# Kernel optimization log

Measured on AMD Instinct MI355X. Metric: run time of the kernel, lower is better.

The kernel has to match this reference:

```python
import jax, jax.numpy as jnp
import numpy as np

D_MODEL = 1024
NUM_HEADS = 16
KEY_DIM = 64
VALUE_DIM = 64
NEG_INF = jnp.float32(-1e30)


def setup_inputs() -> dict:
    key = jax.random.key(0)
    ks = jax.random.split(key, 10)
    B, S = 2, 2048
    lim = 1.0 / np.sqrt(D_MODEL)
    x = jax.random.normal(ks[0], (B, S, D_MODEL), dtype=jnp.float32)
    mask = jnp.ones((B, S), dtype=jnp.int32)  # pad mask: 1 = keep
    # stacked per-head linear params (Linear stores weight as [out, in])
    Wq = jax.random.uniform(ks[1], (NUM_HEADS, KEY_DIM, D_MODEL), jnp.float32, -lim, lim)
    bq = jax.random.uniform(ks[2], (NUM_HEADS, KEY_DIM), jnp.float32, -lim, lim)
    Wk = jax.random.uniform(ks[3], (NUM_HEADS, KEY_DIM, D_MODEL), jnp.float32, -lim, lim)
    bk = jax.random.uniform(ks[4], (NUM_HEADS, KEY_DIM), jnp.float32, -lim, lim)
    Wv = jax.random.uniform(ks[5], (NUM_HEADS, VALUE_DIM, D_MODEL), jnp.float32, -lim, lim)
    bv = jax.random.uniform(ks[6], (NUM_HEADS, VALUE_DIM), jnp.float32, -lim, lim)
    lim_o = 1.0 / np.sqrt(NUM_HEADS * VALUE_DIM)
    Wo = jax.random.uniform(ks[7], (D_MODEL, NUM_HEADS * VALUE_DIM), jnp.float32, -lim_o, lim_o)
    bo = jax.random.uniform(ks[8], (D_MODEL,), jnp.float32, -lim_o, lim_o)
    return {"x": x, "mask": mask, "Wq": Wq, "bq": bq, "Wk": Wk, "bk": bk,
            "Wv": Wv, "bv": bv, "Wo": Wo, "bo": bo}


def _mha(x, mask, Wq, bq, Wk, bk, Wv, bv, Wo, bo):
    B, S, _ = x.shape
    # per-head projections: [B, H, S, k]
    q = jnp.einsum('bsd,hkd->bhsk', x, Wq) + bq[None, :, None, :]
    k = jnp.einsum('bsd,hkd->bhsk', x, Wk) + bk[None, :, None, :]
    v = jnp.einsum('bsd,hvd->bhsv', x, Wv) + bv[None, :, None, :]
    scale = 1.0 / np.sqrt(KEY_DIM).astype(np.float32)
    scores = jnp.einsum('bhik,bhjk->bhij', q, k) * scale  # [B, H, S, S]
    # final mask = causal AND pad-row AND pad-col
    causal = jnp.tril(jnp.ones((S, S), dtype=bool))
    pad = mask.astype(bool)
    final = causal[None, None] & pad[:, None, :, None] & pad[:, None, None, :]
    masked = jnp.where(final, scores, NEG_INF)
    w = jax.nn.softmax(masked, axis=-1)
    w = jnp.where(final, w, 0.0)  # fully-masked rows -> zeros, matching loop impl
    out = jnp.einsum('bhij,bhjv->bhiv', w, v)            # [B, H, S, V]
    concat = out.transpose(0, 2, 1, 3).reshape(B, S, NUM_HEADS * VALUE_DIM)
    return concat @ Wo.T + bo


def reference(x, mask, Wq, bq, Wk, bk, Wv, bv, Wo, bo):
    return _mha(x, mask, Wq, bq, Wk, bk, Wv, bv, Wo, bo)
```

## Files before the change

kernel.cpp:

```cpp
#include <hip/hip_runtime.h>

#define SEQ 2048
#define NH 16
#define HD 64
#define DMODEL 1024

__device__ __forceinline__ unsigned int f2bf(float f) {
  unsigned int u = __float_as_uint(f);
  return ((u + 0x7fffu + ((u >> 16) & 1u)) >> 16) & 0xffffu;
}

__device__ __forceinline__ unsigned int pk2bf(float a, float b) {
  unsigned short ua = __builtin_bit_cast(unsigned short, (__bf16)a);
  unsigned short ub = __builtin_bit_cast(unsigned short, (__bf16)b);
  return (unsigned int)ua | ((unsigned int)ub << 16);
}

typedef __bf16 bf16x8 __attribute__((ext_vector_type(8)));
typedef float f32x4 __attribute__((ext_vector_type(4)));

__device__ __forceinline__ void gl2lds16(const unsigned short* g, unsigned short* l) {
  __builtin_amdgcn_global_load_lds(
      (const __attribute__((address_space(1))) unsigned int*)g,
      (__attribute__((address_space(3))) unsigned int*)l, 16, 0, 0);
}

__global__ __launch_bounds__(256) void cast_all_kernel(
    const float* __restrict__ x, const float* __restrict__ wq,
    const float* __restrict__ wk, const float* __restrict__ wv,
    const float* __restrict__ wo,
    unsigned short* __restrict__ xb, unsigned short* __restrict__ wqb,
    unsigned short* __restrict__ wkb, unsigned short* __restrict__ wvb,
    unsigned short* __restrict__ wob) {
  int idx = blockIdx.x * 256 + threadIdx.x;
  if (idx >= 1048576) return;
  const float* src;
  unsigned short* dst;
  int off;
  if (idx < 524288) {
    src = x; dst = xb; off = idx;
  } else {
    int t = idx - 524288;
    int w = t >> 17;
    off = t & 131071;
    src = (w == 0) ? wq : (w == 1) ? wk : (w == 2) ? wv : wo;
    dst = (w == 0) ? wqb : (w == 1) ? wkb : (w == 2) ? wvb : wob;
  }
  const float4* p = reinterpret_cast<const float4*>(src) + (size_t)off * 2;
  float4 a = p[0], b = p[1];
  uint4 o;
  o.x = f2bf(a.x) | (f2bf(a.y) << 16);
  o.y = f2bf(a.z) | (f2bf(a.w) << 16);
  o.z = f2bf(b.x) | (f2bf(b.y) << 16);
  o.w = f2bf(b.z) | (f2bf(b.w) << 16);
  reinterpret_cast<uint4*>(dst)[off] = o;
}

template <int MODE>
__global__ __launch_bounds__(256) void gemm128(
    const unsigned short* __restrict__ A, const unsigned short* __restrict__ B,
    const float* __restrict__ bias0, const float* __restrict__ bias1,
    const float* __restrict__ bias2, float* __restrict__ Cf,
    unsigned short* __restrict__ Qo, unsigned short* __restrict__ Ko,
    unsigned short* __restrict__ Vto, int Kdim) {
  __shared__ __align__(16) unsigned short As[128 * 64];
  __shared__ __align__(16) unsigned short Bs[128 * 64];
  const int tid = threadIdx.x;
  const int wave = tid >> 6, lane = tid & 63;
  const int wm = wave >> 1, wn = wave & 1;
  const int fr = lane & 15, quad = lane >> 4;
  const int fx = fr & 7;
  const int n0 = blockIdx.x * 128, m0 = blockIdx.y * 128;

  const int srowg = lane >> 3;
  const int schunk = (lane & 7) ^ (srowg & 7);
  const unsigned short* Abase =
      A + (size_t)(m0 + wave * 32 + srowg) * Kdim + schunk * 8;
  const unsigned short* Bbase =
      B + (size_t)(n0 + wave * 32 + srowg) * Kdim + schunk * 8;
  unsigned short* AsW = As + (wave * 32) * 64;
  unsigned short* BsW = Bs + (wave * 32) * 64;

  f32x4 acc[4][4];
#pragma unroll
  for (int mt = 0; mt < 4; ++mt)
#pragma unroll
    for (int nt = 0; nt < 4; ++nt) acc[mt][nt] = f32x4{0.f, 0.f, 0.f, 0.f};

  for (int k0 = 0; k0 < Kdim; k0 += 64) {
#pragma unroll
    for (int t = 0; t < 4; ++t) {
      gl2lds16(Abase + (size_t)(t * 8) * Kdim + k0, AsW + t * 8 * 64);
      gl2lds16(Bbase + (size_t)(t * 8) * Kdim + k0, BsW + t * 8 * 64);
    }
    __syncthreads();
#pragma unroll
    for (int ks = 0; ks < 2; ++ks) {
      bf16x8 af[4], bfv[4];
#pragma unroll
      for (int mt = 0; mt < 4; ++mt)
        af[mt] = *reinterpret_cast<const bf16x8*>(
            As + (wm * 64 + mt * 16 + fr) * 64 + ((ks * 4 + quad) ^ fx) * 8);
#pragma unroll
      for (int nt = 0; nt < 4; ++nt)
        bfv[nt] = *reinterpret_cast<const bf16x8*>(
            Bs + (wn * 64 + nt * 16 + fr) * 64 + ((ks * 4 + quad) ^ fx) * 8);
#pragma unroll
      for (int mt = 0; mt < 4; ++mt)
#pragma unroll
        for (int nt = 0; nt < 4; ++nt)
          acc[mt][nt] = __builtin_amdgcn_mfma_f32_16x16x32_bf16(
              af[mt], bfv[nt], acc[mt][nt], 0, 0, 0);
    }
    __syncthreads();
  }

  if (MODE == 0) {
    const int seg = n0 >> 10;
    const float* bp = (seg == 0) ? bias0 : (seg == 1) ? bias1 : bias2;
    const float scale = (seg == 0) ? 0.1803368809f : 1.0f;
    unsigned short* QK = (seg == 0) ? Qo : Ko;
#pragma unroll
    for (int nt = 0; nt < 4; ++nt) {
      const int c = (n0 + wn * 64 + nt * 16 + fr) & 1023;
      const int h = c >> 6, d = c & 63;
      const float bs = bp[c];
#pragma unroll
      for (int mt = 0; mt < 4; ++mt) {
        const int mbase = m0 + wm * 64 + mt * 16 + quad * 4;
        const int b = mbase >> 11, s0 = mbase & 2047;
        if (seg < 2) {
          unsigned short* dst = QK + (((size_t)(b * NH + h)) * SEQ + s0) * HD + d;
#pragma unroll
          for (int r = 0; r < 4; ++r)
            dst[(size_t)r * HD] = (unsigned short)f2bf((acc[mt][nt][r] + bs) * scale);
        } else {
          uint2 pk;
          pk.x = pk2bf(acc[mt][nt][0] + bs, acc[mt][nt][1] + bs);
          pk.y = pk2bf(acc[mt][nt][2] + bs, acc[mt][nt][3] + bs);
          *reinterpret_cast<uint2*>(
              Vto + (((size_t)(b * NH + h)) * HD + d) * SEQ + s0) = pk;
        }
      }
    }
  } else {
#pragma unroll
    for (int nt = 0; nt < 4; ++nt) {
      const int cg = n0 + wn * 64 + nt * 16 + fr;
      const float bs = bias0[cg];
#pragma unroll
      for (int mt = 0; mt < 4; ++mt) {
        const int mbase = m0 + wm * 64 + mt * 16 + quad * 4;
#pragma unroll
        for (int r = 0; r < 4; ++r)
          Cf[(size_t)(mbase + r) * DMODEL + cg] = acc[mt][nt][r] + bs;
      }
    }
  }
}

__global__ __launch_bounds__(256, 4) void attn_mfma_kernel(
    const unsigned short* __restrict__ Qg, const unsigned short* __restrict__ Kg,
    const unsigned short* __restrict__ Vtg, const int* __restrict__ mask,
    unsigned short* __restrict__ concat) {
  const int w = blockIdx.x >> 8;
  const int c = blockIdx.x & 255;
  const int gg = c >> 5;
  const int bh = c & 31;
  const int ib = (w == 0) ? (31 - gg) : (w == 1) ? gg : (w == 2) ? (23 - gg) : (8 + gg);
  const int b = bh >> 4, h = bh & 15;
  const int tid = threadIdx.x;
  const int wave = tid >> 6, lane = tid & 63;
  const int quad = lane >> 4, fr = lane & 15;
  const int fx = fr & 7;

  __shared__ __align__(16) unsigned short Ks[2][64 * 64];
  __shared__ __align__(16) unsigned short Vts[2][64 * 64];
  __shared__ __align__(16) unsigned short Pt[4][16 * 64];

  const unsigned short* Qb = Qg + ((size_t)bh * SEQ) * HD;
  const unsigned short* Kb = Kg + ((size_t)bh * SEQ) * HD;
  const unsigned short* Vtb = Vtg + ((size_t)bh * HD) * SEQ;
  const int* maskb = mask + b * SEQ;

  bool badl = false;
  {
    const int4* mp4 = reinterpret_cast<const int4*>(maskb);
#pragma unroll
    for (int u = 0; u < 8; ++u) {
      int4 v = mp4[lane * 8 + u];
      badl |= !(v.x && v.y && v.z && v.w);
    }
  }
  const unsigned long long bm = __ballot(badl);

  const int ir = ib * 64 + wave * 16 + fr;
  const bf16x8 q0 = *reinterpret_cast<const bf16x8*>(Qb + (size_t)ir * HD + quad * 8);
  const bf16x8 q1 = *reinterpret_cast<const bf16x8*>(Qb + (size_t)ir * HD + quad * 8 + 32);
  const int padi = maskb[ir];

  f32x4 o[4];
#pragma unroll
  for (int vt = 0; vt < 4; ++vt) o[vt] = f32x4{0.f, 0.f, 0.f, 0.f};
  float mr = -1e20f, lr = 0.f;

  const int srowg = lane >> 3;
  const int schunk = (lane & 7) ^ (srowg & 7);
  const unsigned short* Ksrc = Kb + (size_t)(wave * 16 + srowg) * HD + schunk * 8;
  const unsigned short* Vsrc = Vtb + (size_t)(wave * 16 + srowg) * SEQ + schunk * 8;
  const int cA0 = (quad ^ fx) * 8;
  const int cA1 = ((quad + 4) ^ fx) * 8;
  unsigned short* PtW = Pt[wave];

  {
    unsigned short* KsW = Ks[0] + (wave * 16) * 64;
    unsigned short* VtsW = Vts[0] + (wave * 16) * 64;
#pragma unroll
    for (int t = 0; t < 2; ++t) {
      gl2lds16(Ksrc + (size_t)(t * 8) * HD, KsW + t * 8 * 64);
      gl2lds16(Vsrc + (size_t)(t * 8) * SEQ, VtsW + t * 8 * 64);
    }
  }

  for (int jc = 0; jc <= ib; ++jc) {
    __syncthreads();
    if (jc < ib) {
      const int jn = (jc + 1) * 64;
      unsigned short* KsW = Ks[(jc + 1) & 1] + (wave * 16) * 64;
      unsigned short* VtsW = Vts[(jc + 1) & 1] + (wave * 16) * 64;
#pragma unroll
      for (int t = 0; t < 2; ++t) {
        gl2lds16(Ksrc + (size_t)(jn + t * 8) * HD, KsW + t * 8 * 64);
        gl2lds16(Vsrc + (size_t)(t * 8) * SEQ + jn, VtsW + t * 8 * 64);
      }
    }
    const unsigned short* Kcur = Ks[jc & 1];
    const unsigned short* Vcur = Vts[jc & 1];
    const int j0 = jc * 64;
    const bool tb = ((bm >> (2 * jc)) & 3ull) != 0ull;

    f32x4 st[4];
#pragma unroll
    for (int jt = 0; jt < 4; ++jt) {
      bf16x8 ka0 = *reinterpret_cast<const bf16x8*>(&Kcur[(jt * 16 + fr) * 64 + cA0]);
      bf16x8 ka1 = *reinterpret_cast<const bf16x8*>(&Kcur[(jt * 16 + fr) * 64 + cA1]);
      st[jt] = f32x4{0.f, 0.f, 0.f, 0.f};
      st[jt] = __builtin_amdgcn_mfma_f32_16x16x32_bf16(ka0, q0, st[jt], 0, 0, 0);
      st[jt] = __builtin_amdgcn_mfma_f32_16x16x32_bf16(ka1, q1, st[jt], 0, 0, 0);
    }

    if (tb) {
      const int4* mp = reinterpret_cast<const int4*>(maskb + j0);
#pragma unroll
      for (int jt = 0; jt < 4; ++jt) {
        const int4 mv = mp[jt * 4 + quad];
        if (mv.x == 0) st[jt][0] = -1e30f;
        if (mv.y == 0) st[jt][1] = -1e30f;
        if (mv.z == 0) st[jt][2] = -1e30f;
        if (mv.w == 0) st[jt][3] = -1e30f;
      }
    }
    if (jc == ib) {
#pragma unroll
      for (int jt = 0; jt < 4; ++jt) {
        const int jb = j0 + jt * 16 + quad * 4;
#pragma unroll
        for (int r = 0; r < 4; ++r)
          if (jb + r > ir) st[jt][r] = -1e30f;
      }
    }

    float tmax = -1e30f;
#pragma unroll
    for (int jt = 0; jt < 4; ++jt)
#pragma unroll
      for (int r = 0; r < 4; ++r) tmax = fmaxf(tmax, st[jt][r]);
    tmax = fmaxf(tmax, __shfl_xor(tmax, 16));
    tmax = fmaxf(tmax, __shfl_xor(tmax, 32));
    const bool upd = __ballot(tmax > mr) != 0ull;
    float corr = 1.f;
    if (upd) { const float mn = fmaxf(mr, tmax); corr = __builtin_amdgcn_exp2f(mr - mn); mr = mn; }
    float lloc = 0.f;
#pragma unroll
    for (int jt = 0; jt < 4; ++jt) {
      float p0 = __builtin_amdgcn_exp2f(st[jt][0] - mr);
      float p1 = __builtin_amdgcn_exp2f(st[jt][1] - mr);
      float p2 = __builtin_amdgcn_exp2f(st[jt][2] - mr);
      float p3 = __builtin_amdgcn_exp2f(st[jt][3] - mr);
      lloc += (p0 + p1) + (p2 + p3);
      uint2 pk; pk.x = pk2bf(p0, p1); pk.y = pk2bf(p2, p3);
      const int pc = (2 * jt + (quad >> 1)) ^ fx;
      *reinterpret_cast<uint2*>(&PtW[fr * 64 + pc * 8 + (quad & 1) * 4]) = pk;
    }
    lloc += __shfl_xor(lloc, 16);
    lloc += __shfl_xor(lloc, 32);
    if (upd) {
      lr = lr * corr + lloc;
#pragma unroll
      for (int vt = 0; vt < 4; ++vt) {
        o[vt][0] *= corr; o[vt][1] *= corr; o[vt][2] *= corr; o[vt][3] *= corr;
      }
    } else {
      lr += lloc;
    }

    bf16x8 pa0 = *reinterpret_cast<const bf16x8*>(&PtW[fr * 64 + (quad ^ fx) * 8]);
    bf16x8 pa1 = *reinterpret_cast<const bf16x8*>(&PtW[fr * 64 + ((quad + 4) ^ fx) * 8]);
#pragma unroll
    for (int vt = 0; vt < 4; ++vt) {
      bf16x8 vb0 = *reinterpret_cast<const bf16x8*>(&Vcur[(vt * 16 + fr) * 64 + cA0]);
      bf16x8 vb1 = *reinterpret_cast<const bf16x8*>(&Vcur[(vt * 16 + fr) * 64 + cA1]);
      o[vt] = __builtin_amdgcn_mfma_f32_16x16x32_bf16(vb0, pa0, o[vt], 0, 0, 0);
      o[vt] = __builtin_amdgcn_mfma_f32_16x16x32_bf16(vb1, pa1, o[vt], 0, 0, 0);
    }
  }

  const float inv = (padi != 0 && lr > 0.f) ? 1.f / lr : 0.f;
  unsigned short* orow = concat + ((size_t)(b * SEQ + ir)) * DMODEL + h * HD;
#pragma unroll
  for (int vt = 0; vt < 4; ++vt) {
    uint2 pk;
    pk.x = pk2bf(o[vt][0] * inv, o[vt][1] * inv);
    pk.y = pk2bf(o[vt][2] * inv, o[vt][3] * inv);
    *reinterpret_cast<uint2*>(orow + vt * 16 + quad * 4) = pk;
  }
}

extern "C" void kernel_launch(void* const* d_in, const int* in_sizes, int n_in,
                              void* d_out, int out_size, void* d_ws, size_t ws_size,
                              hipStream_t stream) {
  (void)in_sizes; (void)n_in; (void)out_size;
  const float* x  = (const float*)d_in[0];
  const int* mask = (const int*)d_in[1];
  const float* Wq = (const float*)d_in[2];
  const float* bq = (const float*)d_in[3];
  const float* Wk = (const float*)d_in[4];
  const float* bk = (const float*)d_in[5];
  const float* Wv = (const float*)d_in[6];
  const float* bv = (const float*)d_in[7];
  const float* Wo = (const float*)d_in[8];
  const float* bo = (const float*)d_in[9];
  float* out = (float*)d_out;

  char* ws = (char*)d_ws;
  if (ws_size < (48ull << 20)) return;
  unsigned short* xb  = (unsigned short*)(ws);
  unsigned short* wqb = (unsigned short*)(ws + (8ull  << 20));
  unsigned short* wkb = (unsigned short*)(ws + (10ull << 20));
  unsigned short* wvb = (unsigned short*)(ws + (12ull << 20));
  unsigned short* wob = (unsigned short*)(ws + (14ull << 20));
  unsigned short* Qb  = (unsigned short*)(ws + (16ull << 20));
  unsigned short* Kb  = (unsigned short*)(ws + (24ull << 20));
  unsigned short* Vtb = (unsigned short*)(ws + (32ull << 20));
  unsigned short* cb  = (unsigned short*)(ws + (40ull << 20));

  cast_all_kernel<<<4096, 256, 0, stream>>>(x, Wq, Wk, Wv, Wo, xb, wqb, wkb, wvb, wob);

  gemm128<0><<<dim3(24, 32), 256, 0, stream>>>(xb, wqb, bq, bk, bv,
                                               nullptr, Qb, Kb, Vtb, 1024);

  attn_mfma_kernel<<<1024, 256, 0, stream>>>(Qb, Kb, Vtb, mask, cb);

  gemm128<1><<<dim3(8, 32), 256, 0, stream>>>(cb, wob, bo, nullptr, nullptr,
                                              out, nullptr, nullptr, nullptr, 1024);
}
```

Before: 195.1 us.

## Widen attention KV tiles to 128 and use 64-row tiles for output GEMM

The attention kernel now processes 128 keys per iteration instead of 64. This halves the number of barrier and softmax-rescale steps per query tile and doubles the MFMA work between synchronisations. LDS use doubles and the occupancy hint drops from 4 to 2 blocks per CU, so less latency hiding is possible. The output projection GEMM is templated to 64-row M tiles, doubling its grid to 512 blocks for better CU fill.

```diff
diff --git a/kernel.cpp b/kernel.cpp
--- a/kernel.cpp
+++ b/kernel.cpp
@@ -56,57 +56,59 @@
   reinterpret_cast<uint4*>(dst)[off] = o;
 }
 
-template <int MODE>
+template <int MODE, int TM>
 __global__ __launch_bounds__(256) void gemm128(
     const unsigned short* __restrict__ A, const unsigned short* __restrict__ B,
     const float* __restrict__ bias0, const float* __restrict__ bias1,
     const float* __restrict__ bias2, float* __restrict__ Cf,
     unsigned short* __restrict__ Qo, unsigned short* __restrict__ Ko,
     unsigned short* __restrict__ Vto, int Kdim) {
-  __shared__ __align__(16) unsigned short As[128 * 64];
+  constexpr int MT = TM / 32;
+  __shared__ __align__(16) unsigned short As[TM * 64];
   __shared__ __align__(16) unsigned short Bs[128 * 64];
   const int tid = threadIdx.x;
   const int wave = tid >> 6, lane = tid & 63;
   const int wm = wave >> 1, wn = wave & 1;
   const int fr = lane & 15, quad = lane >> 4;
   const int fx = fr & 7;
-  const int n0 = blockIdx.x * 128, m0 = blockIdx.y * 128;
+  const int n0 = blockIdx.x * 128, m0 = blockIdx.y * TM;
 
   const int srowg = lane >> 3;
   const int schunk = (lane & 7) ^ (srowg & 7);
   const unsigned short* Abase =
-      A + (size_t)(m0 + wave * 32 + srowg) * Kdim + schunk * 8;
+      A + (size_t)(m0 + wave * (TM / 4) + srowg) * Kdim + schunk * 8;
   const unsigned short* Bbase =
       B + (size_t)(n0 + wave * 32 + srowg) * Kdim + schunk * 8;
-  unsigned short* AsW = As + (wave * 32) * 64;
+  unsigned short* AsW = As + (wave * (TM / 4)) * 64;
   unsigned short* BsW = Bs + (wave * 32) * 64;
 
-  f32x4 acc[4][4];
-#pragma unroll
-  for (int mt = 0; mt < 4; ++mt)
+  f32x4 acc[MT][4];
+#pragma unroll
+  for (int mt = 0; mt < MT; ++mt)
 #pragma unroll
     for (int nt = 0; nt < 4; ++nt) acc[mt][nt] = f32x4{0.f, 0.f, 0.f, 0.f};
 
   for (int k0 = 0; k0 < Kdim; k0 += 64) {
 #pragma unroll
-    for (int t = 0; t < 4; ++t) {
+    for (int t = 0; t < TM / 32; ++t)
       gl2lds16(Abase + (size_t)(t * 8) * Kdim + k0, AsW + t * 8 * 64);
+#pragma unroll
+    for (int t = 0; t < 4; ++t)
       gl2lds16(Bbase + (size_t)(t * 8) * Kdim + k0, BsW + t * 8 * 64);
-    }
     __syncthreads();
 #pragma unroll
     for (int ks = 0; ks < 2; ++ks) {
-      bf16x8 af[4], bfv[4];
-#pragma unroll
-      for (int mt = 0; mt < 4; ++mt)
+      bf16x8 af[MT], bfv[4];
+#pragma unroll
+      for (int mt = 0; mt < MT; ++mt)
         af[mt] = *reinterpret_cast<const bf16x8*>(
-            As + (wm * 64 + mt * 16 + fr) * 64 + ((ks * 4 + quad) ^ fx) * 8);
+            As + (wm * (TM / 2) + mt * 16 + fr) * 64 + ((ks * 4 + quad) ^ fx) * 8);
 #pragma unroll
       for (int nt = 0; nt < 4; ++nt)
         bfv[nt] = *reinterpret_cast<const bf16x8*>(
             Bs + (wn * 64 + nt * 16 + fr) * 64 + ((ks * 4 + quad) ^ fx) * 8);
 #pragma unroll
-      for (int mt = 0; mt < 4; ++mt)
+      for (int mt = 0; mt < MT; ++mt)
 #pragma unroll
         for (int nt = 0; nt < 4; ++nt)
           acc[mt][nt] = __builtin_amdgcn_mfma_f32_16x16x32_bf16(
@@ -126,8 +128,8 @@
       const int h = c >> 6, d = c & 63;
       const float bs = bp[c];
 #pragma unroll
-      for (int mt = 0; mt < 4; ++mt) {
-        const int mbase = m0 + wm * 64 + mt * 16 + quad * 4;
+      for (int mt = 0; mt < MT; ++mt) {
+        const int mbase = m0 + wm * (TM / 2) + mt * 16 + quad * 4;
         const int b = mbase >> 11, s0 = mbase & 2047;
         if (seg < 2) {
           unsigned short* dst = QK + (((size_t)(b * NH + h)) * SEQ + s0) * HD + d;
@@ -149,8 +151,8 @@
       const int cg = n0 + wn * 64 + nt * 16 + fr;
       const float bs = bias0[cg];
 #pragma unroll
-      for (int mt = 0; mt < 4; ++mt) {
-        const int mbase = m0 + wm * 64 + mt * 16 + quad * 4;
+      for (int mt = 0; mt < MT; ++mt) {
+        const int mbase = m0 + wm * (TM / 2) + mt * 16 + quad * 4;
 #pragma unroll
         for (int r = 0; r < 4; ++r)
           Cf[(size_t)(mbase + r) * DMODEL + cg] = acc[mt][nt][r] + bs;
@@ -159,7 +161,7 @@
   }
 }
 
-__global__ __launch_bounds__(256, 4) void attn_mfma_kernel(
+__global__ __launch_bounds__(256, 2) void attn_mfma_kernel(
     const unsigned short* __restrict__ Qg, const unsigned short* __restrict__ Kg,
     const unsigned short* __restrict__ Vtg, const int* __restrict__ mask,
     unsigned short* __restrict__ concat) {
@@ -174,9 +176,9 @@
   const int quad = lane >> 4, fr = lane & 15;
   const int fx = fr & 7;
 
-  __shared__ __align__(16) unsigned short Ks[2][64 * 64];
-  __shared__ __align__(16) unsigned short Vts[2][64 * 64];
-  __shared__ __align__(16) unsigned short Pt[4][16 * 64];
+  __shared__ __align__(16) unsigned short Ks[2][128 * 64];
+  __shared__ __align__(16) unsigned short Vts[2][64 * 128];
+  __shared__ __align__(16) unsigned short Pt[4][16 * 128];
 
   const unsigned short* Qb = Qg + ((size_t)bh * SEQ) * HD;
   const unsigned short* Kb = Kg + ((size_t)bh * SEQ) * HD;
@@ -204,44 +206,48 @@
   for (int vt = 0; vt < 4; ++vt) o[vt] = f32x4{0.f, 0.f, 0.f, 0.f};
   float mr = -1e20f, lr = 0.f;
 
-  const int srowg = lane >> 3;
-  const int schunk = (lane & 7) ^ (srowg & 7);
-  const unsigned short* Ksrc = Kb + (size_t)(wave * 16 + srowg) * HD + schunk * 8;
-  const unsigned short* Vsrc = Vtb + (size_t)(wave * 16 + srowg) * SEQ + schunk * 8;
+  const int srow8 = lane >> 3;
+  const int sch8 = (lane & 7) ^ (srow8 & 7);
+  const int srow4 = lane >> 4;
+  const unsigned short* Ksrc = Kb + (size_t)(wave * 32 + srow8) * HD + sch8 * 8;
+  const unsigned short* Vsrc0 = Vtb + (size_t)(wave * 16 + srow4) * SEQ;
   const int cA0 = (quad ^ fx) * 8;
   const int cA1 = ((quad + 4) ^ fx) * 8;
   unsigned short* PtW = Pt[wave];
+  const int nFat = (ib + 2) >> 1;
 
   {
-    unsigned short* KsW = Ks[0] + (wave * 16) * 64;
-    unsigned short* VtsW = Vts[0] + (wave * 16) * 64;
-#pragma unroll
-    for (int t = 0; t < 2; ++t) {
+    unsigned short* KsW = Ks[0] + (wave * 32) * 64;
+    unsigned short* VtsW = Vts[0] + (wave * 16) * 128;
+#pragma unroll
+    for (int t = 0; t < 4; ++t) {
       gl2lds16(Ksrc + (size_t)(t * 8) * HD, KsW + t * 8 * 64);
-      gl2lds16(Vsrc + (size_t)(t * 8) * SEQ, VtsW + t * 8 * 64);
-    }
-  }
-
-  for (int jc = 0; jc <= ib; ++jc) {
+      const int vch = (lane & 15) ^ ((t * 4 + srow4) & 7);
+      gl2lds16(Vsrc0 + (size_t)(t * 4) * SEQ + vch * 8, VtsW + t * 4 * 128);
+    }
+  }
+
+  for (int n = 0; n < nFat; ++n) {
     __syncthreads();
-    if (jc < ib) {
-      const int jn = (jc + 1) * 64;
-      unsigned short* KsW = Ks[(jc + 1) & 1] + (wave * 16) * 64;
-      unsigned short* VtsW = Vts[(jc + 1) & 1] + (wave * 16) * 64;
-#pragma unroll
-      for (int t = 0; t < 2; ++t) {
-        gl2lds16(Ksrc + (size_t)(jn + t * 8) * HD, KsW + t * 8 * 64);
-        gl2lds16(Vsrc + (size_t)(t * 8) * SEQ + jn, VtsW + t * 8 * 64);
-      }
-    }
-    const unsigned short* Kcur = Ks[jc & 1];
-    const unsigned short* Vcur = Vts[jc & 1];
-    const int j0 = jc * 64;
-    const bool tb = ((bm >> (2 * jc)) & 3ull) != 0ull;
-
-    f32x4 st[4];
-#pragma unroll
-    for (int jt = 0; jt < 4; ++jt) {
+    if (n + 1 < nFat) {
+      const int j0n = (n + 1) * 128;
+      unsigned short* KsW = Ks[(n + 1) & 1] + (wave * 32) * 64;
+      unsigned short* VtsW = Vts[(n + 1) & 1] + (wave * 16) * 128;
+#pragma unroll
+      for (int t = 0; t < 4; ++t) {
+        gl2lds16(Ksrc + (size_t)(j0n + t * 8) * HD, KsW + t * 8 * 64);
+        const int vch = (lane & 15) ^ ((t * 4 + srow4) & 7);
+        gl2lds16(Vsrc0 + (size_t)(t * 4) * SEQ + j0n + vch * 8, VtsW + t * 4 * 128);
+      }
+    }
+    const unsigned short* Kcur = Ks[n & 1];
+    const unsigned short* Vcur = Vts[n & 1];
+    const int j0 = n * 128;
+    const int jc0 = 2 * n, jc1 = 2 * n + 1;
+
+    f32x4 st[8];
+#pragma unroll
+    for (int jt = 0; jt < 8; ++jt) {
       bf16x8 ka0 = *reinterpret_cast<const bf16x8*>(&Kcur[(jt * 16 + fr) * 64 + cA0]);
       bf16x8 ka1 = *reinterpret_cast<const bf16x8*>(&Kcur[(jt * 16 + fr) * 64 + cA1]);
       st[jt] = f32x4{0.f, 0.f, 0.f, 0.f};
@@ -249,8 +255,10 @@
       st[jt] = __builtin_amdgcn_mfma_f32_16x16x32_bf16(ka1, q1, st[jt], 0, 0, 0);
     }
 
-    if (tb) {
-      const int4* mp = reinterpret_cast<const int4*>(maskb + j0);
+    const bool tb0 = ((bm >> (2 * jc0)) & 3ull) != 0ull;
+    const bool tb1 = ((bm >> (2 * jc1)) & 3ull) != 0ull;
+    const int4* mp = reinterpret_cast<const int4*>(maskb + j0);
+    if (tb0) {
 #pragma unroll
       for (int jt = 0; jt < 4; ++jt) {
         const int4 mv = mp[jt * 4 + quad];
@@ -260,7 +268,17 @@
         if (mv.w == 0) st[jt][3] = -1e30f;
       }
     }
-    if (jc == ib) {
+    if (tb1) {
+#pragma unroll
+      for (int jt = 4; jt < 8; ++jt) {
+        const int4 mv = mp[jt * 4 + quad];
+        if (mv.x == 0) st[jt][0] = -1e30f;
+        if (mv.y == 0) st[jt][1] = -1e30f;
+        if (mv.z == 0) st[jt][2] = -1e30f;
+        if (mv.w == 0) st[jt][3] = -1e30f;
+      }
+    }
+    if (jc0 >= ib) {
 #pragma unroll
       for (int jt = 0; jt < 4; ++jt) {
         const int jb = j0 + jt * 16 + quad * 4;
@@ -269,12 +287,23 @@
           if (jb + r > ir) st[jt][r] = -1e30f;
       }
     }
-
-    float tmax = -1e30f;
-#pragma unroll
-    for (int jt = 0; jt < 4; ++jt)
-#pragma unroll
-      for (int r = 0; r < 4; ++r) tmax = fmaxf(tmax, st[jt][r]);
+    if (jc1 >= ib) {
+#pragma unroll
+      for (int jt = 4; jt < 8; ++jt) {
+        const int jb = j0 + jt * 16 + quad * 4;
+#pragma unroll
+        for (int r = 0; r < 4; ++r)
+          if (jb + r > ir) st[jt][r] = -1e30f;
+      }
+    }
+
+    float mj[8];
+#pragma unroll
+    for (int jt = 0; jt < 8; ++jt)
+      mj[jt] = fmaxf(fmaxf(st[jt][0], st[jt][1]), fmaxf(st[jt][2], st[jt][3]));
+    float t01 = fmaxf(mj[0], mj[1]), t23 = fmaxf(mj[2], mj[3]);
+    float t45 = fmaxf(mj[4], mj[5]), t67 = fmaxf(mj[6], mj[7]);
+    float tmax = fmaxf(fmaxf(t01, t23), fmaxf(t45, t67));
     tmax = fmaxf(tmax, __shfl_xor(tmax, 16));
     tmax = fmaxf(tmax, __shfl_xor(tmax, 32));
     const bool upd = __ballot(tmax > mr) != 0ull;
@@ -282,7 +311,7 @@
     if (upd) { const float mn = fmaxf(mr, tmax); corr = __builtin_amdgcn_exp2f(mr - mn); mr = mn; }
     float lloc = 0.f;
 #pragma unroll
-    for (int jt = 0; jt < 4; ++jt) {
+    for (int jt = 0; jt < 8; ++jt) {
       float p0 = __builtin_amdgcn_exp2f(st[jt][0] - mr);
       float p1 = __builtin_amdgcn_exp2f(st[jt][1] - mr);
       float p2 = __builtin_amdgcn_exp2f(st[jt][2] - mr);
@@ -290,7 +319,7 @@
       lloc += (p0 + p1) + (p2 + p3);
       uint2 pk; pk.x = pk2bf(p0, p1); pk.y = pk2bf(p2, p3);
       const int pc = (2 * jt + (quad >> 1)) ^ fx;
-      *reinterpret_cast<uint2*>(&PtW[fr * 64 + pc * 8 + (quad & 1) * 4]) = pk;
+      *reinterpret_cast<uint2*>(&PtW[fr * 128 + pc * 8 + (quad & 1) * 4]) = pk;
     }
     lloc += __shfl_xor(lloc, 16);
     lloc += __shfl_xor(lloc, 32);
@@ -304,14 +333,20 @@
       lr += lloc;
     }
 
-    bf16x8 pa0 = *reinterpret_cast<const bf16x8*>(&PtW[fr * 64 + (quad ^ fx) * 8]);
-    bf16x8 pa1 = *reinterpret_cast<const bf16x8*>(&PtW[fr * 64 + ((quad + 4) ^ fx) * 8]);
+    bf16x8 pa0 = *reinterpret_cast<const bf16x8*>(&PtW[fr * 128 + ((0 + quad) ^ fx) * 8]);
+    bf16x8 pa1 = *reinterpret_cast<const bf16x8*>(&PtW[fr * 128 + ((4 + quad) ^ fx) * 8]);
+    bf16x8 pa2 = *reinterpret_cast<const bf16x8*>(&PtW[fr * 128 + ((8 + quad) ^ fx) * 8]);
+    bf16x8 pa3 = *reinterpret_cast<const bf16x8*>(&PtW[fr * 128 + ((12 + quad) ^ fx) * 8]);
 #pragma unroll
     for (int vt = 0; vt < 4; ++vt) {
-      bf16x8 vb0 = *reinterpret_cast<const bf16x8*>(&Vcur[(vt * 16 + fr) * 64 + cA0]);
-      bf16x8 vb1 = *reinterpret_cast<const bf16x8*>(&Vcur[(vt * 16 + fr) * 64 + cA1]);
+      bf16x8 vb0 = *reinterpret_cast<const bf16x8*>(&Vcur[(vt * 16 + fr) * 128 + ((0 + quad) ^ fx) * 8]);
+      bf16x8 vb1 = *reinterpret_cast<const bf16x8*>(&Vcur[(vt * 16 + fr) * 128 + ((4 + quad) ^ fx) * 8]);
+      bf16x8 vb2 = *reinterpret_cast<const bf16x8*>(&Vcur[(vt * 16 + fr) * 128 + ((8 + quad) ^ fx) * 8]);
+      bf16x8 vb3 = *reinterpret_cast<const bf16x8*>(&Vcur[(vt * 16 + fr) * 128 + ((12 + quad) ^ fx) * 8]);
       o[vt] = __builtin_amdgcn_mfma_f32_16x16x32_bf16(vb0, pa0, o[vt], 0, 0, 0);
       o[vt] = __builtin_amdgcn_mfma_f32_16x16x32_bf16(vb1, pa1, o[vt], 0, 0, 0);
+      o[vt] = __builtin_amdgcn_mfma_f32_16x16x32_bf16(vb2, pa2, o[vt], 0, 0, 0);
+      o[vt] = __builtin_amdgcn_mfma_f32_16x16x32_bf16(vb3, pa3, o[vt], 0, 0, 0);
     }
   }
 
@@ -356,11 +391,11 @@
 
   cast_all_kernel<<<4096, 256, 0, stream>>>(x, Wq, Wk, Wv, Wo, xb, wqb, wkb, wvb, wob);
 
-  gemm128<0><<<dim3(24, 32), 256, 0, stream>>>(xb, wqb, bq, bk, bv,
-                                               nullptr, Qb, Kb, Vtb, 1024);
+  gemm128<0, 128><<<dim3(24, 32), 256, 0, stream>>>(xb, wqb, bq, bk, bv,
+                                                    nullptr, Qb, Kb, Vtb, 1024);
 
   attn_mfma_kernel<<<1024, 256, 0, stream>>>(Qb, Kb, Vtb, mask, cb);
 
-  gemm128<1><<<dim3(8, 32), 256, 0, stream>>>(cb, wob, bo, nullptr, nullptr,
-                                              out, nullptr, nullptr, nullptr, 1024);
-}
+  gemm128<1, 64><<<dim3(8, 64), 256, 0, stream>>>(cb, wob, bo, nullptr, nullptr,
+                                                  out, nullptr, nullptr, nullptr, 1024);
+}
```

After: 202.2 us. +3.7%, slower.
